# Performance work log

Hardware: AMD Instinct MI355X
Metric: run time of the kernel (lower is better)

## Reference

```python
import jax, jax.numpy as jnp
import numpy as np

B, N, C, E = 512, 1000, 50, 128
H, D = 8, 16          # head_num, qkv_dim; H*D == E
CLIP = 10.0           # logit_clipping
NEG = -1e9


def setup_inputs() -> dict:
    key = jax.random.key(0)
    ks = jax.random.split(key, 20)
    f = lambda i, shape, s=1.0: jax.random.normal(ks[i], shape, dtype=jnp.float32) * s
    w = 0.05  # small weight scale so tanh/softmax stay in a sane range
    return dict(
        depot_embedding=f(0, (B, 1, E)),
        cluster_embedding=f(1, (B, C, E)),
        current_embedding=f(2, (B, 1, E)),
        node_embeddings=f(3, (B, N, E)),
        aug_context_embedding=f(4, (B, 1, 4 * E)),
        cluster_guidance_embedding=f(5, (B, 1, E)),
        Wq=f(6, (3 * E, E), w), Wk=f(7, (E, E), w), Wv=f(8, (E, E), w), Wks=f(9, (E, E), w),
        mha_Wq=f(10, (E, H * D), w), mha_Wk=f(11, (E, H * D), w),
        mha_Wv=f(12, (E, H * D), w), mha_Wo=f(13, (H * D, E), w),
        is_new_cluster=jax.random.bernoulli(ks[14], 0.5, (B,)),
        mask=jax.random.bernoulli(ks[15], 0.5, (B, 1, N)),
        cluster_mask=jax.random.bernoulli(ks[16], 0.5, (B, 1, N)),
        visited_cluster_mask=jax.random.bernoulli(ks[17], 0.3, (B, 1, C)),
        cluster_guidance=jax.random.randint(ks[18], (B,), 0, C),
        step=1,
    )


def reference(depot_embedding, cluster_embedding, current_embedding, node_embeddings,
              aug_context_embedding, cluster_guidance_embedding,
              Wq, Wk, Wv, Wks, mha_Wq, mha_Wk, mha_Wv, mha_Wo,
              is_new_cluster, mask, cluster_mask, visited_cluster_mask,
              cluster_guidance, step):
    # step > 0 path: init_* buffers come from the passed-in tensors.
    b, n, e = node_embeddings.shape
    c = cluster_embedding.shape[1]

    def unvisit_embed(m):  # m: [B,1,N] bool, True = visited
        mm = m[:, 0, :, None]                                    # [B,N,1]
        return jnp.where(mm, 0.0, node_embeddings).sum(axis=1, keepdims=True) / n  # [B,1,E]

    # --- new-cluster branch, computed full-batch and selected with where ---
    unvisit_mean = unvisit_embed(mask)                            # [B,1,E]
    context = jnp.concatenate([unvisit_mean, current_embedding, depot_embedding], axis=2)  # [B,1,3E]
    q = context @ Wq                                              # [B,1,E]
    k = cluster_embedding @ Wk                                    # [B,C,E]
    v = cluster_embedding @ Wv                                    # [B,C,E]
    pk = cluster_embedding @ Wks                                  # [B,C,E]

    # if all non-depot clusters visited, unmask cluster 0; else mask it
    all_visited = jnp.all(visited_cluster_mask[:, 0, 1:], axis=1)  # [B]
    vcm = visited_cluster_mask.at[:, 0, 0].set(~all_visited)      # [B,1,C]

    # multi-head glimpse attention
    qh = (q @ mha_Wq).reshape(b, 1, H, D).transpose(0, 2, 1, 3)   # [B,H,1,D]
    kh = (k @ mha_Wk).reshape(b, c, H, D).transpose(0, 2, 1, 3)   # [B,H,C,D]
    vh = (v @ mha_Wv).reshape(b, c, H, D).transpose(0, 2, 1, 3)   # [B,H,C,D]
    scores = jnp.einsum('bhqd,bhkd->bhqk', qh, kh) / jnp.sqrt(jnp.float32(D))
    scores = jnp.where(vcm[:, None, :, :], NEG, scores)           # mask over keys
    attn = jax.nn.softmax(scores, axis=-1)
    glimpse = jnp.einsum('bhqk,bhkd->bhqd', attn, vh)             # [B,H,1,D]
    glimpse = glimpse.transpose(0, 2, 1, 3).reshape(b, 1, H * D) @ mha_Wo  # [B,1,E]

    logit = jnp.einsum('bqe,bce->bqc', glimpse, pk)[:, 0, :] / jnp.sqrt(jnp.float32(e))  # [B,C]
    logit = jnp.tanh(logit) * CLIP
    logit = jnp.where(vcm[:, 0, :], NEG, logit)
    log_p = jax.nn.log_softmax(logit, axis=1)                     # [B,C]

    new_guidance = jnp.argmax(log_p, axis=1)                      # greedy select_mode
    new_guid_embed = jnp.take_along_axis(cluster_embedding, new_guidance[:, None, None], axis=1)  # [B,1,E]

    unvisit_cluster = unvisit_embed(mask | cluster_mask)          # [B,1,E]
    new_aug = jnp.concatenate([unvisit_cluster, current_embedding, new_guid_embed, depot_embedding], axis=2)  # [B,1,4E]

    # --- scatter back: keep old values for rows without a new cluster ---
    is_new = is_new_cluster
    sel3 = is_new[:, None, None]
    aug_out = jnp.where(sel3, new_aug, aug_context_embedding)
    guid_embed_out = jnp.where(sel3, new_guid_embed, cluster_guidance_embedding)
    guid_out = jnp.where(is_new, new_guidance.astype(cluster_guidance.dtype), cluster_guidance)
    clu_prob = jnp.where(is_new[:, None], log_p, 0.0)
    return aug_out, guid_embed_out, guid_out, clu_prob
```

## Files before the change

kernel.cpp:

```cpp
#include <hip/hip_runtime.h>
#include <hip/hip_bf16.h>
#include <math.h>

#define BB 512
#define NN 1000
#define CC 50
#define EE 128
#define HH 8
#define DD 16
#define NEGV (-1000000000.0f)

#define O_AUG 0
#define O_GE  (512*512)
#define O_G   (O_GE + 512*128)
#define O_CP  (O_G + 512)

typedef float vf4 __attribute__((ext_vector_type(4)));

__global__ __launch_bounds__(512) void prep(
    const float* __restrict__ node, const int* __restrict__ mask,
    const int* __restrict__ cmask,
    const float* __restrict__ Wq, const float* __restrict__ Wk,
    const float* __restrict__ Wv, const float* __restrict__ Wks,
    const float* __restrict__ mWq, const float* __restrict__ mWk,
    const float* __restrict__ mWv, const float* __restrict__ Wo,
    float* __restrict__ um, float* __restrict__ uc,
    float* __restrict__ Wqh, float* __restrict__ Wkh,
    float* __restrict__ Wvh, float* __restrict__ WoKs)
{
    int t = threadIdx.x;
    if (blockIdx.x < 512) {
        __shared__ float2 w[1000];
        __shared__ vf4 s1[16][32];
        __shared__ vf4 s2[16][32];
        int b = blockIdx.x;
        const int* mb = mask  + b * NN;
        const int* cb = cmask + b * NN;
        for (int n = t; n < NN; n += 512) {
            int m1 = mb[n];
            int m2 = m1 | cb[n];
            w[n] = make_float2(m1 ? 0.f : 1.f, m2 ? 0.f : 1.f);
        }
        __syncthreads();

        int v = t & 31, r = t >> 5;
        const vf4* np = (const vf4*)(node + (size_t)b * NN * EE);
        vf4 a1 = {0.f, 0.f, 0.f, 0.f};
        vf4 a2 = {0.f, 0.f, 0.f, 0.f};
        int n = r;
        for (; n + 48 < NN; n += 64) {
            vf4 x0 = __builtin_nontemporal_load(np + (n     ) * 32 + v);
            vf4 x1 = __builtin_nontemporal_load(np + (n + 16) * 32 + v);
            vf4 x2 = __builtin_nontemporal_load(np + (n + 32) * 32 + v);
            vf4 x3 = __builtin_nontemporal_load(np + (n + 48) * 32 + v);
            float2 w0 = w[n], w1 = w[n + 16], w2 = w[n + 32], w3 = w[n + 48];
            a1 += x0 * w0.x; a2 += x0 * w0.y;
            a1 += x1 * w1.x; a2 += x1 * w1.y;
            a1 += x2 * w2.x; a2 += x2 * w2.y;
            a1 += x3 * w3.x; a2 += x3 * w3.y;
        }
        for (; n < NN; n += 16) {
            vf4 x = __builtin_nontemporal_load(np + n * 32 + v);
            float2 ww = w[n];
            a1 += x * ww.x;
            a2 += x * ww.y;
        }
        s1[r][v] = a1;
        s2[r][v] = a2;
        __syncthreads();
        if (t < 128) {
            const float* f1 = (const float*)s1;
            const float* f2 = (const float*)s2;
            float x1 = 0.f, x2 = 0.f;
#pragma unroll
            for (int rr = 0; rr < 16; ++rr) {
                x1 += f1[rr * 128 + t];
                x2 += f2[rr * 128 + t];
            }
            um[b * 128 + t] = x1 * (1.0f / (float)NN);
            uc[b * 128 + t] = x2 * (1.0f / (float)NN);
        }
    } else {
        int wb = blockIdx.x - 512;
        int r0 = wb * 16;
        int sub = t >> 7;
        int e = t & 127;
        const float* A; const float* Bm; float* O; int rb; float sc; bool tb;
        if (r0 < 384)      { A = Wq; Bm = mWq; O = Wqh;  rb = r0;       sc = 0.25f; tb = false; }
        else if (r0 < 512) { A = Wk; Bm = mWk; O = Wkh;  rb = r0 - 384; sc = 1.0f;  tb = false; }
        else if (r0 < 640) { A = Wv; Bm = mWv; O = Wvh;  rb = r0 - 512; sc = 1.0f;  tb = false; }
        else               { A = Wo; Bm = Wks; O = WoKs; rb = r0 - 640; sc = 1.0f;  tb = true;  }
        float acc[4] = {0.f, 0.f, 0.f, 0.f};
        if (!tb) {
            for (int i = 0; i < 128; ++i) {
                float bv = Bm[i * 128 + e];
#pragma unroll
                for (int k = 0; k < 4; ++k)
                    acc[k] = fmaf(A[(rb + sub + 4 * k) * 128 + i], bv, acc[k]);
            }
        } else {
            for (int i = 0; i < 128; ++i) {
                float bv = Bm[e * 128 + i];
#pragma unroll
                for (int k = 0; k < 4; ++k)
                    acc[k] = fmaf(A[(rb + sub + 4 * k) * 128 + i], bv, acc[k]);
            }
        }
#pragma unroll
        for (int k = 0; k < 4; ++k)
            O[(rb + sub + 4 * k) * 128 + e] = acc[k] * sc;
    }
}

__global__ __launch_bounds__(256) void fused_attn(
    const float* __restrict__ depot, const float* __restrict__ ce,
    const float* __restrict__ cur,   const float* __restrict__ augc,
    const float* __restrict__ cge,
    const int* __restrict__ isnew_p, const int* __restrict__ vmask,
    const int* __restrict__ guid,
    const float* __restrict__ um,    const float* __restrict__ uc,
    const float* __restrict__ Wqh,   const float* __restrict__ Wkh,
    const float* __restrict__ Wvh,   const float* __restrict__ WoKs,
    float* __restrict__ out)
{
    int b = blockIdx.x;
    int t = threadIdx.x;

    __shared__ float sT[128 * 57];
    __shared__ float sctx[384];
    __shared__ float sqh[128];
    __shared__ float spq[2][128];
    __shared__ float sU[8 * 128];
    __shared__ float sattn[8 * 64];
    __shared__ float sp[8 * 136];
    __shared__ float sg[128];
    __shared__ float sr[128];
    __shared__ float slog[64];
    __shared__ int   svcm[64];
    __shared__ float s_m, s_lse;
    __shared__ int   s_arg;

    const float* ceb = ce + (size_t)b * CC * EE;

    for (int u = t; u < CC * EE; u += 256) {
        int j = u >> 7, i = u & 127;
        sT[i * 57 + j] = ceb[u];
    }
    if (t < 128) {
        sctx[t]       = um[b * 128 + t];
        sctx[128 + t] = cur[b * 128 + t];
        sctx[256 + t] = depot[b * 128 + t];
    }
    if (t < 64) svcm[t] = (t < CC) ? vmask[b * CC + t] : 1;
    __syncthreads();

    if (t < 64) {
        int pred = (t >= 1 && t < CC) ? (svcm[t] != 0) : 1;
        int allv = __all(pred);
        if (t == 0) svcm[0] = !allv;
    }
    {
        int e = t & 127, half = t >> 7;
        int i0 = half * 192;
        float acc = 0.f;
#pragma unroll 8
        for (int i = 0; i < 192; ++i)
            acc = fmaf(sctx[i0 + i], Wqh[(i0 + i) * 128 + e], acc);
        spq[half][e] = acc;
    }
    __syncthreads();
    if (t < 128) sqh[t] = spq[0][t] + spq[1][t];
    __syncthreads();

    for (int u = t; u < 8 * 128; u += 256) {
        int h = u >> 7, i = u & 127;
        const float* wk = Wkh + i * 128 + h * 16;
        const float* q  = sqh + h * 16;
        float acc = 0.f;
#pragma unroll
        for (int d = 0; d < 16; ++d) acc = fmaf(wk[d], q[d], acc);
        sU[u] = acc;
    }
    __syncthreads();

    for (int u = t; u < 8 * CC; u += 256) {
        int h = u / CC, j = u - h * CC;
        float acc = 0.f;
#pragma unroll 8
        for (int i = 0; i < 128; ++i)
            acc = fmaf(sT[i * 57 + j], sU[h * 128 + i], acc);
        sattn[h * 64 + j] = svcm[j] ? NEGV : acc;
    }
    __syncthreads();

    {
        int h = t >> 5, l = t & 31;
        float s0 = sattn[h * 64 + l];
        float s1v = (l < CC - 32) ? sattn[h * 64 + l + 32] : -INFINITY;
        float m = fmaxf(s0, s1v);
#pragma unroll
        for (int off = 16; off >= 1; off >>= 1)
            m = fmaxf(m, __shfl_xor(m, off, 32));
        float e0 = expf(s0 - m);
        float e1 = (l < CC - 32) ? expf(s1v - m) : 0.f;
        float ssum = e0 + e1;
#pragma unroll
        for (int off = 16; off >= 1; off >>= 1)
            ssum += __shfl_xor(ssum, off, 32);
        float inv = 1.0f / ssum;
        sattn[h * 64 + l] = e0 * inv;
        if (l < CC - 32) sattn[h * 64 + l + 32] = e1 * inv;
    }
    __syncthreads();

    for (int u = t; u < 8 * 128; u += 256) {
        int h = u >> 7, i = u & 127;
        float acc = 0.f;
#pragma unroll
        for (int j = 0; j < CC; ++j)
            acc = fmaf(sattn[h * 64 + j], sT[i * 57 + j], acc);
        sp[h * 136 + i] = acc;
    }
    __syncthreads();

    if (t < 128) {
        int h = t >> 4;
        float acc = 0.f;
#pragma unroll 8
        for (int i = 0; i < 128; ++i)
            acc = fmaf(sp[h * 136 + i], Wvh[i * 128 + t], acc);
        sg[t] = acc;
    }
    __syncthreads();

    if (t < 128) {
        float acc = 0.f;
#pragma unroll 8
        for (int g = 0; g < 128; ++g)
            acc = fmaf(sg[g], WoKs[g * 128 + t], acc);
        sr[t] = acc;
    }
    __syncthreads();

    if (t < 64) {
        if (t < CC) {
            float acc = 0.f;
#pragma unroll 8
            for (int i = 0; i < 128; ++i)
                acc = fmaf(sT[i * 57 + t], sr[i], acc);
            float l = tanhf(acc * 0.08838834764831845f) * 10.0f;
            slog[t] = svcm[t] ? NEGV : l;
        } else {
            slog[t] = NEGV;
        }
    }
    __syncthreads();

    if (t < 64) {
        float val = (t < CC) ? slog[t] : -INFINITY;
        int idx = t;
#pragma unroll
        for (int off = 32; off >= 1; off >>= 1) {
            float ov = __shfl_xor(val, off, 64);
            int   oi = __shfl_xor(idx, off, 64);
            if (ov > val || (ov == val && oi < idx)) { val = ov; idx = oi; }
        }
        float m = val;
        float ex = (t < CC) ? expf(slog[t] - m) : 0.f;
#pragma unroll
        for (int off = 32; off >= 1; off >>= 1)
            ex += __shfl_xor(ex, off, 64);
        if (t == 0) { s_m = m; s_arg = idx; s_lse = logf(ex); }
    }
    __syncthreads();

    bool nw = (isnew_p[b] != 0);
    int  g  = s_arg;
    if (t == 0) {
        out[O_G + b] = nw ? (float)g : (float)guid[b];
    }
    if (t < 128) {
        float nge = sT[t * 57 + g];
        const float* ac = augc + (size_t)b * 512;
        float a0 = nw ? uc[b * 128 + t]    : ac[t];
        float a1 = nw ? cur[b * 128 + t]   : ac[128 + t];
        float a2 = nw ? nge                : ac[256 + t];
        float a3 = nw ? depot[b * 128 + t] : ac[384 + t];
        float* ao = out + O_AUG + (size_t)b * 512;
        ao[t] = a0; ao[128 + t] = a1; ao[256 + t] = a2; ao[384 + t] = a3;
        out[O_GE + b * 128 + t] = nw ? nge : cge[b * 128 + t];
    }
    if (t < CC) {
        out[O_CP + b * CC + t] = nw ? ((slog[t] - s_m) - s_lse) : 0.0f;
    }
}

extern "C" void kernel_launch(void* const* d_in, const int* in_sizes, int n_in,
                              void* d_out, int out_size, void* d_ws, size_t ws_size,
                              hipStream_t stream) {
    const float* depot = (const float*)d_in[0];
    const float* ce    = (const float*)d_in[1];
    const float* cur   = (const float*)d_in[2];
    const float* node  = (const float*)d_in[3];
    const float* augc  = (const float*)d_in[4];
    const float* cge   = (const float*)d_in[5];
    const float* Wq    = (const float*)d_in[6];
    const float* Wk    = (const float*)d_in[7];
    const float* Wv    = (const float*)d_in[8];
    const float* Wks   = (const float*)d_in[9];
    const float* mWq   = (const float*)d_in[10];
    const float* mWk   = (const float*)d_in[11];
    const float* mWv   = (const float*)d_in[12];
    const float* mWo   = (const float*)d_in[13];
    const int*   isnew = (const int*)d_in[14];
    const int*   mask  = (const int*)d_in[15];
    const int*   cmask = (const int*)d_in[16];
    const int*   vmask = (const int*)d_in[17];
    const int*   guid  = (const int*)d_in[18];
    float* out = (float*)d_out;

    float* ws   = (float*)d_ws;
    float* um   = ws;
    float* uc   = um   + 512 * 128;
    float* Wqh  = uc   + 512 * 128;
    float* Wkh  = Wqh  + 384 * 128;
    float* Wvh  = Wkh  + 128 * 128;
    float* WoKs = Wvh  + 128 * 128;

    prep<<<560, 512, 0, stream>>>(node, mask, cmask,
                                  Wq, Wk, Wv, Wks, mWq, mWk, mWv, mWo,
                                  um, uc, Wqh, Wkh, Wvh, WoKs);
    fused_attn<<<512, 256, 0, stream>>>(depot, ce, cur, augc, cge,
                                        isnew, vmask, guid,
                                        um, uc, Wqh, Wkh, Wvh, WoKs, out);
}
```

Baseline: 417.3 us.

## Fuse node mean reduction into attention kernel and split weight prep

Moves the per-batch masked mean over node embeddings into the attention kernel, which now runs 512 threads per block. This removes the global round-trip for the um/uc buffers. Weight folding becomes its own small kernel launched first. The streaming node read now shares a block with the attention work and overlaps the ce transpose load, but the block carries more shared memory and several stages leave half the threads idle.

```diff
diff --git a/kernel.cpp b/kernel.cpp
--- a/kernel.cpp
+++ b/kernel.cpp
@@ -17,32 +17,107 @@
 
 typedef float vf4 __attribute__((ext_vector_type(4)));
 
-__global__ __launch_bounds__(512) void prep(
-    const float* __restrict__ node, const int* __restrict__ mask,
-    const int* __restrict__ cmask,
+__global__ __launch_bounds__(512) void wprep(
     const float* __restrict__ Wq, const float* __restrict__ Wk,
     const float* __restrict__ Wv, const float* __restrict__ Wks,
     const float* __restrict__ mWq, const float* __restrict__ mWk,
     const float* __restrict__ mWv, const float* __restrict__ Wo,
-    float* __restrict__ um, float* __restrict__ uc,
     float* __restrict__ Wqh, float* __restrict__ Wkh,
     float* __restrict__ Wvh, float* __restrict__ WoKs)
 {
+    int t   = threadIdx.x;
+    int r0  = blockIdx.x * 16;
+    int sub = t >> 7;
+    int e   = t & 127;
+    const float* A; const float* Bm; float* O; int rb; float sc; bool tb;
+    if (r0 < 384)      { A = Wq; Bm = mWq; O = Wqh;  rb = r0;       sc = 0.25f; tb = false; }
+    else if (r0 < 512) { A = Wk; Bm = mWk; O = Wkh;  rb = r0 - 384; sc = 1.0f;  tb = false; }
+    else if (r0 < 640) { A = Wv; Bm = mWv; O = Wvh;  rb = r0 - 512; sc = 1.0f;  tb = false; }
+    else               { A = Wo; Bm = Wks; O = WoKs; rb = r0 - 640; sc = 1.0f;  tb = true;  }
+    float acc[4] = {0.f, 0.f, 0.f, 0.f};
+    if (!tb) {
+        for (int i = 0; i < 128; ++i) {
+            float bv = Bm[i * 128 + e];
+#pragma unroll
+            for (int k = 0; k < 4; ++k)
+                acc[k] = fmaf(A[(rb + sub + 4 * k) * 128 + i], bv, acc[k]);
+        }
+    } else {
+        for (int i = 0; i < 128; ++i) {
+            float bv = Bm[e * 128 + i];
+#pragma unroll
+            for (int k = 0; k < 4; ++k)
+                acc[k] = fmaf(A[(rb + sub + 4 * k) * 128 + i], bv, acc[k]);
+        }
+    }
+#pragma unroll
+    for (int k = 0; k < 4; ++k)
+        O[(rb + sub + 4 * k) * 128 + e] = acc[k] * sc;
+}
+
+__global__ __launch_bounds__(512) void mega(
+    const float* __restrict__ node,  const int* __restrict__ mask,
+    const int* __restrict__ cmask,
+    const float* __restrict__ depot, const float* __restrict__ ce,
+    const float* __restrict__ cur,   const float* __restrict__ augc,
+    const float* __restrict__ cge,
+    const int* __restrict__ isnew_p, const int* __restrict__ vmask,
+    const int* __restrict__ guid,
+    const float* __restrict__ Wqh,   const float* __restrict__ Wkh,
+    const float* __restrict__ Wvh,   const float* __restrict__ WoKs,
+    float* __restrict__ out)
+{
+    int b = blockIdx.x;
     int t = threadIdx.x;
-    if (blockIdx.x < 512) {
-        __shared__ float2 w[1000];
-        __shared__ vf4 s1[16][32];
-        __shared__ vf4 s2[16][32];
-        int b = blockIdx.x;
-        const int* mb = mask  + b * NN;
-        const int* cb = cmask + b * NN;
-        for (int n = t; n < NN; n += 512) {
-            int m1 = mb[n];
-            int m2 = m1 | cb[n];
-            w[n] = make_float2(m1 ? 0.f : 1.f, m2 ? 0.f : 1.f);
-        }
-        __syncthreads();
-
+
+    __shared__ float  sT[128 * 57];
+    __shared__ float2 w[1000];
+    __shared__ vf4    s1[16][32];
+    __shared__ vf4    s2[16][32];
+    __shared__ float  sctx[384];
+    __shared__ float  suc[128];
+    __shared__ float  spq[4][128];
+    __shared__ float  sqh[128];
+    __shared__ float  sU[8 * 128];
+    __shared__ float  sattn[8 * 64];
+    __shared__ float  sp[8 * 136];
+    __shared__ float  sg[128];
+    __shared__ float  sr[128];
+    __shared__ float  slog[64];
+    __shared__ int    svcm[64];
+    __shared__ float  s_m, s_lse;
+    __shared__ int    s_arg;
+
+    const int* mb = mask  + b * NN;
+    const int* cb = cmask + b * NN;
+    for (int n = t; n < NN; n += 512) {
+        int m1 = mb[n];
+        int m2 = m1 | cb[n];
+        w[n] = make_float2(m1 ? 0.f : 1.f, m2 ? 0.f : 1.f);
+    }
+    const float* ceb = ce + (size_t)b * CC * EE;
+    for (int u = t; u < CC * EE; u += 512) {
+        int j = u >> 7, i = u & 127;
+        sT[i * 57 + j] = ceb[u];
+    }
+    if (t >= 128 && t < 256) {
+        int e = t - 128;
+        sctx[128 + e] = cur[b * 128 + e];
+        sctx[256 + e] = depot[b * 128 + e];
+    }
+    if (t >= 256 && t < 320) {
+        int j = t - 256;
+        svcm[j] = (j < CC) ? vmask[b * CC + j] : 1;
+    }
+    __syncthreads();
+
+    if (t < 64) {
+        int pred = (t >= 1 && t < CC) ? (svcm[t] != 0) : 1;
+        int allv = __all(pred);
+        if (t == 0) svcm[0] = !allv;
+    }
+
+    {
         int v = t & 31, r = t >> 5;
         const vf4* np = (const vf4*)(node + (size_t)b * NN * EE);
         vf4 a1 = {0.f, 0.f, 0.f, 0.f};
@@ -67,112 +142,36 @@
         }
         s1[r][v] = a1;
         s2[r][v] = a2;
-        __syncthreads();
-        if (t < 128) {
-            const float* f1 = (const float*)s1;
-            const float* f2 = (const float*)s2;
-            float x1 = 0.f, x2 = 0.f;
-#pragma unroll
-            for (int rr = 0; rr < 16; ++rr) {
-                x1 += f1[rr * 128 + t];
-                x2 += f2[rr * 128 + t];
-            }
-            um[b * 128 + t] = x1 * (1.0f / (float)NN);
-            uc[b * 128 + t] = x2 * (1.0f / (float)NN);
-        }
-    } else {
-        int wb = blockIdx.x - 512;
-        int r0 = wb * 16;
-        int sub = t >> 7;
-        int e = t & 127;
-        const float* A; const float* Bm; float* O; int rb; float sc; bool tb;
-        if (r0 < 384)      { A = Wq; Bm = mWq; O = Wqh;  rb = r0;       sc = 0.25f; tb = false; }
-        else if (r0 < 512) { A = Wk; Bm = mWk; O = Wkh;  rb = r0 - 384; sc = 1.0f;  tb = false; }
-        else if (r0 < 640) { A = Wv; Bm = mWv; O = Wvh;  rb = r0 - 512; sc = 1.0f;  tb = false; }
-        else               { A = Wo; Bm = Wks; O = WoKs; rb = r0 - 640; sc = 1.0f;  tb = true;  }
-        float acc[4] = {0.f, 0.f, 0.f, 0.f};
-        if (!tb) {
-            for (int i = 0; i < 128; ++i) {
-                float bv = Bm[i * 128 + e];
-#pragma unroll
-                for (int k = 0; k < 4; ++k)
-                    acc[k] = fmaf(A[(rb + sub + 4 * k) * 128 + i], bv, acc[k]);
-            }
-        } else {
-            for (int i = 0; i < 128; ++i) {
-                float bv = Bm[e * 128 + i];
-#pragma unroll
-                for (int k = 0; k < 4; ++k)
-                    acc[k] = fmaf(A[(rb + sub + 4 * k) * 128 + i], bv, acc[k]);
-            }
-        }
-#pragma unroll
-        for (int k = 0; k < 4; ++k)
-            O[(rb + sub + 4 * k) * 128 + e] = acc[k] * sc;
-    }
-}
-
-__global__ __launch_bounds__(256) void fused_attn(
-    const float* __restrict__ depot, const float* __restrict__ ce,
-    const float* __restrict__ cur,   const float* __restrict__ augc,
-    const float* __restrict__ cge,
-    const int* __restrict__ isnew_p, const int* __restrict__ vmask,
-    const int* __restrict__ guid,
-    const float* __restrict__ um,    const float* __restrict__ uc,
-    const float* __restrict__ Wqh,   const float* __restrict__ Wkh,
-    const float* __restrict__ Wvh,   const float* __restrict__ WoKs,
-    float* __restrict__ out)
-{
-    int b = blockIdx.x;
-    int t = threadIdx.x;
-
-    __shared__ float sT[128 * 57];
-    __shared__ float sctx[384];
-    __shared__ float sqh[128];
-    __shared__ float spq[2][128];
-    __shared__ float sU[8 * 128];
-    __shared__ float sattn[8 * 64];
-    __shared__ float sp[8 * 136];
-    __shared__ float sg[128];
-    __shared__ float sr[128];
-    __shared__ float slog[64];
-    __shared__ int   svcm[64];
-    __shared__ float s_m, s_lse;
-    __shared__ int   s_arg;
-
-    const float* ceb = ce + (size_t)b * CC * EE;
-
-    for (int u = t; u < CC * EE; u += 256) {
-        int j = u >> 7, i = u & 127;
-        sT[i * 57 + j] = ceb[u];
-    }
+    }
+    __syncthreads();
     if (t < 128) {
-        sctx[t]       = um[b * 128 + t];
-        sctx[128 + t] = cur[b * 128 + t];
-        sctx[256 + t] = depot[b * 128 + t];
-    }
-    if (t < 64) svcm[t] = (t < CC) ? vmask[b * CC + t] : 1;
-    __syncthreads();
-
-    if (t < 64) {
-        int pred = (t >= 1 && t < CC) ? (svcm[t] != 0) : 1;
-        int allv = __all(pred);
-        if (t == 0) svcm[0] = !allv;
-    }
+        const float* f1 = (const float*)s1;
+        const float* f2 = (const float*)s2;
+        float x1 = 0.f, x2 = 0.f;
+#pragma unroll
+        for (int rr = 0; rr < 16; ++rr) {
+            x1 += f1[rr * 128 + t];
+            x2 += f2[rr * 128 + t];
+        }
+        sctx[t] = x1 * (1.0f / (float)NN);
+        suc[t]  = x2 * (1.0f / (float)NN);
+    }
+    __syncthreads();
+
     {
-        int e = t & 127, half = t >> 7;
-        int i0 = half * 192;
-        float acc = 0.f;
-#pragma unroll 8
-        for (int i = 0; i < 192; ++i)
+        int e = t & 127, q4 = t >> 7;
+        int i0 = q4 * 96;
+        float acc = 0.f;
+#pragma unroll 8
+        for (int i = 0; i < 96; ++i)
             acc = fmaf(sctx[i0 + i], Wqh[(i0 + i) * 128 + e], acc);
-        spq[half][e] = acc;
-    }
-    __syncthreads();
-    if (t < 128) sqh[t] = spq[0][t] + spq[1][t];
-    __syncthreads();
-
-    for (int u = t; u < 8 * 128; u += 256) {
+        spq[q4][e] = acc;
+    }
+    __syncthreads();
+    if (t < 128) sqh[t] = (spq[0][t] + spq[1][t]) + (spq[2][t] + spq[3][t]);
+    __syncthreads();
+
+    for (int u = t; u < 8 * 128; u += 512) {
         int h = u >> 7, i = u & 127;
         const float* wk = Wkh + i * 128 + h * 16;
         const float* q  = sqh + h * 16;
@@ -183,8 +182,8 @@
     }
     __syncthreads();
 
-    for (int u = t; u < 8 * CC; u += 256) {
-        int h = u / CC, j = u - h * CC;
+    if (t < 8 * CC) {
+        int h = t / CC, j = t - h * CC;
         float acc = 0.f;
 #pragma unroll 8
         for (int i = 0; i < 128; ++i)
@@ -193,9 +192,9 @@
     }
     __syncthreads();
 
-    {
+    if (t < 256) {
         int h = t >> 5, l = t & 31;
-        float s0 = sattn[h * 64 + l];
+        float s0  = sattn[h * 64 + l];
         float s1v = (l < CC - 32) ? sattn[h * 64 + l + 32] : -INFINITY;
         float m = fmaxf(s0, s1v);
 #pragma unroll
@@ -213,7 +212,7 @@
     }
     __syncthreads();
 
-    for (int u = t; u < 8 * 128; u += 256) {
+    for (int u = t; u < 8 * 128; u += 512) {
         int h = u >> 7, i = u & 127;
         float acc = 0.f;
 #pragma unroll
@@ -282,16 +281,17 @@
     if (t < 128) {
         float nge = sT[t * 57 + g];
         const float* ac = augc + (size_t)b * 512;
-        float a0 = nw ? uc[b * 128 + t]    : ac[t];
-        float a1 = nw ? cur[b * 128 + t]   : ac[128 + t];
+        float a0 = nw ? suc[t]             : ac[t];
+        float a1 = nw ? sctx[128 + t]      : ac[128 + t];
         float a2 = nw ? nge                : ac[256 + t];
-        float a3 = nw ? depot[b * 128 + t] : ac[384 + t];
+        float a3 = nw ? sctx[256 + t]      : ac[384 + t];
         float* ao = out + O_AUG + (size_t)b * 512;
         ao[t] = a0; ao[128 + t] = a1; ao[256 + t] = a2; ao[384 + t] = a3;
         out[O_GE + b * 128 + t] = nw ? nge : cge[b * 128 + t];
     }
-    if (t < CC) {
-        out[O_CP + b * CC + t] = nw ? ((slog[t] - s_m) - s_lse) : 0.0f;
+    if (t >= 128 && t < 128 + CC) {
+        int j = t - 128;
+        out[O_CP + b * CC + j] = nw ? ((slog[j] - s_m) - s_lse) : 0.0f;
     }
 }
 
@@ -320,17 +320,15 @@
     float* out = (float*)d_out;
 
     float* ws   = (float*)d_ws;
-    float* um   = ws;
-    float* uc   = um   + 512 * 128;
-    float* Wqh  = uc   + 512 * 128;
+    float* Wqh  = ws;
     float* Wkh  = Wqh  + 384 * 128;
     float* Wvh  = Wkh  + 128 * 128;
     float* WoKs = Wvh  + 128 * 128;
 
-    prep<<<560, 512, 0, stream>>>(node, mask, cmask,
-                                  Wq, Wk, Wv, Wks, mWq, mWk, mWv, mWo,
-                                  um, uc, Wqh, Wkh, Wvh, WoKs);
-    fused_attn<<<512, 256, 0, stream>>>(depot, ce, cur, augc, cge,
-                                        isnew, vmask, guid,
-                                        um, uc, Wqh, Wkh, Wvh, WoKs, out);
+    wprep<<<48, 512, 0, stream>>>(Wq, Wk, Wv, Wks, mWq, mWk, mWv, mWo,
+                                  Wqh, Wkh, Wvh, WoKs);
+    mega<<<512, 512, 0, stream>>>(node, mask, cmask,
+                                  depot, ce, cur, augc, cge,
+                                  isnew, vmask, guid,
+                                  Wqh, Wkh, Wvh, WoKs, out);
 }
```

After: 414.6 us. No clear change (-0.6%).
